# Performance work log

Hardware: AMD Instinct MI355X
Metric: run time of the kernel (lower is better)

## Reference

```python
import jax, jax.numpy as jnp
import numpy as np

B, T, C, H = 2, 2048, 1024, 16
D = C // H  # head dim = 64


def setup_inputs() -> dict:
    key = jax.random.key(0)
    ks = jax.random.split(key, 9)
    s = 1.0 / np.sqrt(C)
    x = jax.random.normal(ks[0], (B, T, C), dtype=jnp.float32)
    # causal lower-triangular mask, broadcast over heads: [B, 1, T, T]
    attn_mask = jnp.broadcast_to(jnp.tril(jnp.ones((T, T), dtype=jnp.int32)), (B, 1, T, T))
    Wq = jax.random.normal(ks[1], (C, C), dtype=jnp.float32) * s
    Wk = jax.random.normal(ks[2], (C, C), dtype=jnp.float32) * s
    Wv = jax.random.normal(ks[3], (C, C), dtype=jnp.float32) * s
    Wo = jax.random.normal(ks[4], (C, C), dtype=jnp.float32) * s
    bq = jax.random.normal(ks[5], (C,), dtype=jnp.float32) * s
    bk = jax.random.normal(ks[6], (C,), dtype=jnp.float32) * s
    bv = jax.random.normal(ks[7], (C,), dtype=jnp.float32) * s
    bo = jax.random.normal(ks[8], (C,), dtype=jnp.float32) * s
    return {"x": x, "attn_mask": attn_mask, "Wq": Wq, "bq": bq, "Wk": Wk, "bk": bk,
            "Wv": Wv, "bv": bv, "Wo": Wo, "bo": bo}


def reference(x, attn_mask, Wq, bq, Wk, bk, Wv, bv, Wo, bo):
    # Q/K/V projections: nn.Linear applies x @ W^T + b
    def split_heads(t):  # [B,T,C] -> [B,H,T,D]
        return t.reshape(B, T, H, D).transpose(0, 2, 1, 3)

    q = split_heads(x @ Wq.T + bq)
    k = split_heads(x @ Wk.T + bk)
    v = split_heads(x @ Wv.T + bv)

    scale = 1.0 / np.sqrt(D)
    att = jnp.einsum('bhqd,bhkd->bhqk', q, k) * scale  # [B,H,T,T]
    att = jnp.where(attn_mask[:, :, :T, :T] == 0, -jnp.inf, att)
    att = jax.nn.softmax(att, axis=-1)
    # dropout p=0.0 -> identity
    y = jnp.einsum('bhqk,bhkd->bhqd', att, v)  # [B,H,T,D]
    y = y.transpose(0, 2, 1, 3).reshape(B, T, C)
    return y @ Wo.T + bo
```

## Files before the change

kernel.cpp:

```cpp
#include <hip/hip_runtime.h>
#include <hip/hip_bf16.h>

#define B_ 2
#define T_ 2048
#define C_ 1024
#define H_ 16
#define D_ 64
#define BT_ (B_ * T_)
#define S3_ 3072

typedef __bf16 bf16x8 __attribute__((ext_vector_type(8)));
typedef short short8 __attribute__((ext_vector_type(8)));
typedef float f32x4 __attribute__((ext_vector_type(4)));

__device__ inline bf16x8 ld_frag_bf(const short* p) {
    short8 s = *(const short8*)p;
    return __builtin_bit_cast(bf16x8, s);
}
__device__ inline short f2bf(float f) {
    union { float f; unsigned u; } x;
    x.f = f;
    unsigned r = x.u + 0x7fff + ((x.u >> 16) & 1);
    return (short)(r >> 16);
}
__device__ inline void st_out(short* p, float v) { *p = f2bf(v); }
__device__ inline void st_out(float* p, float v) { *p = v; }

__device__ inline void async16(const void* g, void* l) {
    __builtin_amdgcn_global_load_lds(
        (const __attribute__((address_space(1))) unsigned*)g,
        (__attribute__((address_space(3))) unsigned*)l, 16, 0, 0);
}

__global__ __launch_bounds__(256) void conv_inputs(
    const float* __restrict__ x,
    const float* __restrict__ Wq, const float* __restrict__ Wk,
    const float* __restrict__ Wv, const float* __restrict__ Wo,
    short* __restrict__ xb, short* __restrict__ Wqkvb, short* __restrict__ Wob)
{
    size_t e = ((size_t)blockIdx.x * 256 + threadIdx.x) * 8;
    int r = (int)(e >> 20);
    size_t off = e & ((1u << 20) - 1);
    const float* src; short* dst;
    if (r < 4)      { src = x + e;  dst = xb + e; }
    else if (r < 7) { src = (r == 4 ? Wq : r == 5 ? Wk : Wv) + off;
                      dst = Wqkvb + ((size_t)(r - 4) << 20) + off; }
    else            { src = Wo + off; dst = Wob + off; }
    f32x4 a = *(const f32x4*)src;
    f32x4 b = *(const f32x4*)(src + 4);
    short8 s;
#pragma unroll
    for (int i = 0; i < 4; ++i) { s[i] = f2bf(a[i]); s[i + 4] = f2bf(b[i]); }
    *(short8*)dst = s;
}

template <typename OT>
__global__ __launch_bounds__(256) void gemm_m97(
    const short* __restrict__ A, int lda,
    const short* __restrict__ Wb,
    const float* __restrict__ b0, const float* __restrict__ b1,
    const float* __restrict__ b2,
    OT* __restrict__ Out, int ldo)
{
    constexpr int K = 1024;
    __shared__ __align__(16) short Bs[128 * 32];
    __shared__ __align__(16) short As[128 * 32];

    const int tid = threadIdx.x;
    const int w = tid >> 6, l = tid & 63;
    const int c = l & 15, qd = l >> 4;
    const int m0 = blockIdx.y * 128, n0 = blockIdx.x * 128;
    const int wm = w >> 1, wn = w & 1;

    const float* bias = (n0 < 1024) ? b0 : (n0 < 2048 ? b1 : b2);

    f32x4 acc[4][4] = {};

    for (int k0 = 0; k0 < K; k0 += 32) {
#pragma unroll
        for (int p = 0; p < 2; ++p) {
            int row = p * 64 + w * 16 + (l >> 2);
            async16(Wb + (size_t)(n0 + row) * K + k0 + (l & 3) * 8,
                    Bs + p * 2048 + w * 512 + l * 8);
            async16(A + (size_t)(m0 + row) * lda + k0 + (l & 3) * 8,
                    As + p * 2048 + w * 512 + l * 8);
        }
        __syncthreads();

        bf16x8 af[4], bfr[4];
#pragma unroll
        for (int i = 0; i < 4; ++i) {
            af[i]  = ld_frag_bf(As + (wm * 64 + i * 16 + c) * 32 + qd * 8);
            bfr[i] = ld_frag_bf(Bs + (wn * 64 + i * 16 + c) * 32 + qd * 8);
        }
#pragma unroll
        for (int i = 0; i < 4; ++i)
#pragma unroll
            for (int j = 0; j < 4; ++j)
                acc[i][j] = __builtin_amdgcn_mfma_f32_16x16x32_bf16(af[i], bfr[j], acc[i][j], 0, 0, 0);
        __syncthreads();
    }

#pragma unroll
    for (int i = 0; i < 4; ++i)
#pragma unroll
        for (int j = 0; j < 4; ++j) {
            int n = n0 + wn * 64 + j * 16 + c;
            float bv = bias[n & 1023];
#pragma unroll
            for (int r = 0; r < 4; ++r) {
                int m = m0 + wm * 64 + i * 16 + qd * 4 + r;
                st_out(Out + (size_t)m * ldo + n, acc[i][j][r] + bv);
            }
        }
}

__global__ __launch_bounds__(256) void attn_flash4(short* __restrict__ QKV)
{
    __shared__ __align__(16) short Ksm[2][64 * 64];
    __shared__ __align__(16) short Vsm[2][64 * 72];
    __shared__ __align__(16) short Psm[4][16 * 72];

    const int tid = threadIdx.x;
    const int w = tid >> 6, l = tid & 63;
    const int c = l & 15, qd = l >> 4;
    const int pair = blockIdx.x;
    const int bh = blockIdx.y;
    const int b = bh >> 4, h = bh & 15;
    const int sw = c & 7;

    short* Qbase = QKV + (size_t)b * T_ * S3_ + h * 64;
    const short* Kbase = Qbase + 1024;
    const short* Vbase = Qbase + 2048;

#pragma unroll 1
    for (int seg = 0; seg < 2; ++seg) {
        const int qt = (seg == 0) ? pair : 31 - pair;
        const int q0 = qt * 64, wq0 = q0 + w * 16;

        bf16x8 aq0 = ld_frag_bf(Qbase + (size_t)(wq0 + c) * S3_ + qd * 8);
        bf16x8 aq1 = ld_frag_bf(Qbase + (size_t)(wq0 + c) * S3_ + 32 + qd * 8);

        f32x4 o[4] = {};
        float lrow[4] = {0.f, 0.f, 0.f, 0.f};

        {
#pragma unroll
            for (int p = 0; p < 2; ++p) {
                int row = p * 32 + w * 8 + (l >> 3);
                int srcC = (l & 7) ^ (row & 7);
                async16(Kbase + (size_t)row * S3_ + srcC * 8,
                        &Ksm[0][row * 64 + (l & 7) * 8]);
            }
            const short* g = Vbase + (size_t)l * S3_ + w * 16;
            short8 v0 = *(const short8*)g;
            short8 v1 = *(const short8*)(g + 8);
#pragma unroll
            for (int e = 0; e < 8; ++e) {
                Vsm[0][(w * 16 + e) * 72 + l]     = v0[e];
                Vsm[0][(w * 16 + 8 + e) * 72 + l] = v1[e];
            }
        }
        __syncthreads();

#pragma unroll 1
        for (int kt = 0; kt <= qt; ++kt) {
            const int cur = kt & 1;
            const int k0 = kt * 64;

            short8 nv0, nv1;
            if (kt < qt) {
#pragma unroll
                for (int p = 0; p < 2; ++p) {
                    int row = p * 32 + w * 8 + (l >> 3);
                    int srcC = (l & 7) ^ (row & 7);
                    async16(Kbase + (size_t)(k0 + 64 + row) * S3_ + srcC * 8,
                            &Ksm[1 - cur][row * 64 + (l & 7) * 8]);
                }
                const short* g = Vbase + (size_t)(k0 + 64 + l) * S3_ + w * 16;
                nv0 = *(const short8*)g;
                nv1 = *(const short8*)(g + 8);
            }

            f32x4 s[4];
#pragma unroll
            for (int j = 0; j < 4; ++j) {
                s[j] = (f32x4){0.f, 0.f, 0.f, 0.f};
                const short* kr = &Ksm[cur][(j * 16 + c) * 64];
                bf16x8 kb0 = ld_frag_bf(kr + (qd ^ sw) * 8);
                bf16x8 kb1 = ld_frag_bf(kr + (qd ^ 4 ^ sw) * 8);
                s[j] = __builtin_amdgcn_mfma_f32_16x16x32_bf16(aq0, kb0, s[j], 0, 0, 0);
                s[j] = __builtin_amdgcn_mfma_f32_16x16x32_bf16(aq1, kb1, s[j], 0, 0, 0);
            }

            const bool diag = (kt == qt);
            float p_[4][4];
#pragma unroll
            for (int r = 0; r < 4; ++r) {
                const int qrow = wq0 + qd * 4 + r;
                float acc = 0.f;
#pragma unroll
                for (int j = 0; j < 4; ++j) {
                    float p = __expf(fmaf(s[j][r], 0.125f, -8.0f));
                    if (diag && (k0 + j * 16 + c > qrow)) p = 0.f;
                    p_[r][j] = p;
                    acc += p;
                }
                lrow[r] += acc;
            }

            short* P = Psm[w];
#pragma unroll
            for (int r = 0; r < 4; ++r)
#pragma unroll
                for (int j = 0; j < 4; ++j)
                    P[(qd * 4 + r) * 72 + j * 16 + c] = f2bf(p_[r][j]);

            if (kt < qt) {
#pragma unroll
                for (int e = 0; e < 8; ++e) {
                    Vsm[1 - cur][(w * 16 + e) * 72 + l]     = nv0[e];
                    Vsm[1 - cur][(w * 16 + 8 + e) * 72 + l] = nv1[e];
                }
            }

            bf16x8 pa0 = ld_frag_bf(P + c * 72 + qd * 8);
            bf16x8 pa1 = ld_frag_bf(P + c * 72 + 32 + qd * 8);
#pragma unroll
            for (int j = 0; j < 4; ++j) {
                bf16x8 vb0 = ld_frag_bf(&Vsm[cur][(j * 16 + c) * 72 + qd * 8]);
                bf16x8 vb1 = ld_frag_bf(&Vsm[cur][(j * 16 + c) * 72 + 32 + qd * 8]);
                o[j] = __builtin_amdgcn_mfma_f32_16x16x32_bf16(pa0, vb0, o[j], 0, 0, 0);
                o[j] = __builtin_amdgcn_mfma_f32_16x16x32_bf16(pa1, vb1, o[j], 0, 0, 0);
            }
            __syncthreads();
        }

        float inv[4];
#pragma unroll
        for (int r = 0; r < 4; ++r) {
            float s = lrow[r];
            s += __shfl_xor(s, 1);
            s += __shfl_xor(s, 2);
            s += __shfl_xor(s, 4);
            s += __shfl_xor(s, 8);
            inv[r] = 1.0f / s;
        }

#pragma unroll
        for (int j = 0; j < 4; ++j)
#pragma unroll
            for (int r = 0; r < 4; ++r) {
                int qrow = wq0 + qd * 4 + r;
                Qbase[(size_t)qrow * S3_ + j * 16 + c] = f2bf(o[j][r] * inv[r]);
            }
    }
}

extern "C" void kernel_launch(void* const* d_in, const int* in_sizes, int n_in,
                              void* d_out, int out_size, void* d_ws, size_t ws_size,
                              hipStream_t stream)
{
    const float* x  = (const float*)d_in[0];
    const float* Wq = (const float*)d_in[2];
    const float* bq = (const float*)d_in[3];
    const float* Wk = (const float*)d_in[4];
    const float* bk = (const float*)d_in[5];
    const float* Wv = (const float*)d_in[6];
    const float* bv = (const float*)d_in[7];
    const float* Wo = (const float*)d_in[8];
    const float* bo = (const float*)d_in[9];
    float* out = (float*)d_out;

    short* QKVs  = (short*)d_ws;
    short* Wqkvb = QKVs + (size_t)BT_ * S3_;
    short* Wob   = Wqkvb + (size_t)S3_ * C_;
    short* xb    = (short*)d_out;

    conv_inputs<<<4096, 256, 0, stream>>>(x, Wq, Wk, Wv, Wo, xb, Wqkvb, Wob);
    gemm_m97<short><<<dim3(S3_ / 128, BT_ / 128), 256, 0, stream>>>(
        xb, C_, Wqkvb, bq, bk, bv, QKVs, S3_);
    attn_flash4<<<dim3(16, B_ * H_), 256, 0, stream>>>(QKVs);
    gemm_m97<float><<<dim3(C_ / 128, BT_ / 128), 256, 0, stream>>>(
        QKVs, S3_, Wob, bo, bo, bo, out, C_);
}
```

Baseline: 227.6 us.

## Pre-transpose V, async-load it in attention, split mask path, retile output GEMM

A new kernel writes V in a transposed layout to a scratch area inside the output buffer. The attention kernel can then load V tiles with async 16-byte copies into swizzled shared memory, replacing the register-staged scatter transpose it did on every tile. The kernel also uses a remapped 1-D grid to group heads, and evaluates the causal mask only on the diagonal tile. The output projection moves to a new 128x64-tile GEMM, which doubles its block count, at the cost of one extra launch and an extra pass over V.

Measured after the change: 210.4 us. -7.5%, faster.

```diff
diff --git a/kernel.cpp b/kernel.cpp
--- a/kernel.cpp
+++ b/kernel.cpp
@@ -115,28 +115,122 @@
         }
 }
 
-__global__ __launch_bounds__(256) void attn_flash4(short* __restrict__ QKV)
-{
-    __shared__ __align__(16) short Ksm[2][64 * 64];
-    __shared__ __align__(16) short Vsm[2][64 * 72];
-    __shared__ __align__(16) short Psm[4][16 * 72];
+template <typename OT>
+__global__ __launch_bounds__(256) void gemm_n64(
+    const short* __restrict__ A, int lda,
+    const short* __restrict__ Wb, const float* __restrict__ bias,
+    OT* __restrict__ Out, int ldo)
+{
+    constexpr int K = 1024;
+    __shared__ __align__(16) short Bs[64 * 32];
+    __shared__ __align__(16) short As[128 * 32];
 
     const int tid = threadIdx.x;
     const int w = tid >> 6, l = tid & 63;
     const int c = l & 15, qd = l >> 4;
-    const int pair = blockIdx.x;
-    const int bh = blockIdx.y;
+    const int m0 = blockIdx.y * 128, n0 = blockIdx.x * 64;
+    const int wm = w >> 1, wn = w & 1;
+
+    f32x4 acc[4][2] = {};
+
+    for (int k0 = 0; k0 < K; k0 += 32) {
+        {
+            int row = w * 16 + (l >> 2);
+            async16(Wb + (size_t)(n0 + row) * K + k0 + (l & 3) * 8,
+                    Bs + w * 512 + l * 8);
+        }
+#pragma unroll
+        for (int p = 0; p < 2; ++p) {
+            int row = p * 64 + w * 16 + (l >> 2);
+            async16(A + (size_t)(m0 + row) * lda + k0 + (l & 3) * 8,
+                    As + p * 2048 + w * 512 + l * 8);
+        }
+        __syncthreads();
+
+        bf16x8 af[4], bfr[2];
+#pragma unroll
+        for (int i = 0; i < 4; ++i)
+            af[i] = ld_frag_bf(As + (wm * 64 + i * 16 + c) * 32 + qd * 8);
+#pragma unroll
+        for (int j = 0; j < 2; ++j)
+            bfr[j] = ld_frag_bf(Bs + (wn * 32 + j * 16 + c) * 32 + qd * 8);
+#pragma unroll
+        for (int i = 0; i < 4; ++i)
+#pragma unroll
+            for (int j = 0; j < 2; ++j)
+                acc[i][j] = __builtin_amdgcn_mfma_f32_16x16x32_bf16(af[i], bfr[j], acc[i][j], 0, 0, 0);
+        __syncthreads();
+    }
+
+#pragma unroll
+    for (int i = 0; i < 4; ++i)
+#pragma unroll
+        for (int j = 0; j < 2; ++j) {
+            int n = n0 + wn * 32 + j * 16 + c;
+            float bv = bias[n];
+#pragma unroll
+            for (int r = 0; r < 4; ++r) {
+                int m = m0 + wm * 64 + i * 16 + qd * 4 + r;
+                st_out(Out + (size_t)m * ldo + n, acc[i][j][r] + bv);
+            }
+        }
+}
+
+__global__ __launch_bounds__(256) void transpose_v(
+    const short* __restrict__ QKV, short* __restrict__ VT)
+{
+    __shared__ short Tm[64 * 80];
+    const int t = threadIdx.x;
+    const int kt = blockIdx.x, bh = blockIdx.y;
+    const int b = bh >> 4, h = bh & 15;
+    const short* Vg = QKV + (size_t)b * T_ * S3_ + 2048 + h * 64;
+
+    {
+        int key = t >> 2, dc = (t & 3) * 16;
+        const short* g = Vg + (size_t)(kt * 64 + key) * S3_ + dc;
+        short8 a = *(const short8*)g;
+        short8 c8 = *(const short8*)(g + 8);
+#pragma unroll
+        for (int e = 0; e < 8; ++e) {
+            Tm[(dc + e) * 80 + key]     = a[e];
+            Tm[(dc + 8 + e) * 80 + key] = c8[e];
+        }
+    }
+    __syncthreads();
+    {
+        int d = t >> 2, kc = (t & 3) * 16;
+        short8 w0 = *(const short8*)&Tm[d * 80 + kc];
+        short8 w1 = *(const short8*)&Tm[d * 80 + kc + 8];
+        short* o = VT + ((size_t)bh * 64 + d) * T_ + kt * 64 + kc;
+        *(short8*)o = w0;
+        *(short8*)(o + 8) = w1;
+    }
+}
+
+__global__ __launch_bounds__(256) void attn_flash5(
+    short* __restrict__ QKV, const short* __restrict__ VT)
+{
+    __shared__ __align__(16) short Ksm[2][64 * 64];
+    __shared__ __align__(16) short Vsm[2][64 * 64];
+    __shared__ __align__(16) short Psm[4][16 * 72];
+
+    const int tid = threadIdx.x;
+    const int w = tid >> 6, l = tid & 63;
+    const int c = l & 15, qd = l >> 4;
+    const int id = blockIdx.x;
+    const int bh = (id & 7) * 4 + ((id >> 3) & 3);
+    const int pair = id >> 5;
     const int b = bh >> 4, h = bh & 15;
     const int sw = c & 7;
 
     short* Qbase = QKV + (size_t)b * T_ * S3_ + h * 64;
     const short* Kbase = Qbase + 1024;
-    const short* Vbase = Qbase + 2048;
+    const short* VTb = VT + (size_t)bh * 64 * T_;
 
 #pragma unroll 1
     for (int seg = 0; seg < 2; ++seg) {
-        const int qt = (seg == 0) ? pair : 31 - pair;
-        const int q0 = qt * 64, wq0 = q0 + w * 16;
+        const int qt = seg ? (31 - pair) : pair;
+        const int wq0 = qt * 64 + w * 16;
 
         bf16x8 aq0 = ld_frag_bf(Qbase + (size_t)(wq0 + c) * S3_ + qd * 8);
         bf16x8 aq1 = ld_frag_bf(Qbase + (size_t)(wq0 + c) * S3_ + 32 + qd * 8);
@@ -144,22 +238,14 @@
         f32x4 o[4] = {};
         float lrow[4] = {0.f, 0.f, 0.f, 0.f};
 
-        {
-#pragma unroll
-            for (int p = 0; p < 2; ++p) {
-                int row = p * 32 + w * 8 + (l >> 3);
-                int srcC = (l & 7) ^ (row & 7);
-                async16(Kbase + (size_t)row * S3_ + srcC * 8,
-                        &Ksm[0][row * 64 + (l & 7) * 8]);
-            }
-            const short* g = Vbase + (size_t)l * S3_ + w * 16;
-            short8 v0 = *(const short8*)g;
-            short8 v1 = *(const short8*)(g + 8);
-#pragma unroll
-            for (int e = 0; e < 8; ++e) {
-                Vsm[0][(w * 16 + e) * 72 + l]     = v0[e];
-                Vsm[0][(w * 16 + 8 + e) * 72 + l] = v1[e];
-            }
+#pragma unroll
+        for (int p = 0; p < 2; ++p) {
+            int row = p * 32 + w * 8 + (l >> 3);
+            int srcC = (l & 7) ^ (row & 7);
+            async16(Kbase + (size_t)row * S3_ + srcC * 8,
+                    &Ksm[0][row * 64 + (l & 7) * 8]);
+            async16(VTb + (size_t)row * T_ + srcC * 8,
+                    &Vsm[0][row * 64 + (l & 7) * 8]);
         }
         __syncthreads();
 
@@ -168,7 +254,6 @@
             const int cur = kt & 1;
             const int k0 = kt * 64;
 
-            short8 nv0, nv1;
             if (kt < qt) {
 #pragma unroll
                 for (int p = 0; p < 2; ++p) {
@@ -176,10 +261,9 @@
                     int srcC = (l & 7) ^ (row & 7);
                     async16(Kbase + (size_t)(k0 + 64 + row) * S3_ + srcC * 8,
                             &Ksm[1 - cur][row * 64 + (l & 7) * 8]);
+                    async16(VTb + (size_t)row * T_ + k0 + 64 + srcC * 8,
+                            &Vsm[1 - cur][row * 64 + (l & 7) * 8]);
                 }
-                const short* g = Vbase + (size_t)(k0 + 64 + l) * S3_ + w * 16;
-                nv0 = *(const short8*)g;
-                nv1 = *(const short8*)(g + 8);
             }
 
             f32x4 s[4];
@@ -188,25 +272,38 @@
                 s[j] = (f32x4){0.f, 0.f, 0.f, 0.f};
                 const short* kr = &Ksm[cur][(j * 16 + c) * 64];
                 bf16x8 kb0 = ld_frag_bf(kr + (qd ^ sw) * 8);
-                bf16x8 kb1 = ld_frag_bf(kr + (qd ^ 4 ^ sw) * 8);
+                bf16x8 kb1 = ld_frag_bf(kr + ((qd ^ 4) ^ sw) * 8);
                 s[j] = __builtin_amdgcn_mfma_f32_16x16x32_bf16(aq0, kb0, s[j], 0, 0, 0);
                 s[j] = __builtin_amdgcn_mfma_f32_16x16x32_bf16(aq1, kb1, s[j], 0, 0, 0);
             }
 
-            const bool diag = (kt == qt);
             float p_[4][4];
-#pragma unroll
-            for (int r = 0; r < 4; ++r) {
-                const int qrow = wq0 + qd * 4 + r;
-                float acc = 0.f;
-#pragma unroll
-                for (int j = 0; j < 4; ++j) {
-                    float p = __expf(fmaf(s[j][r], 0.125f, -8.0f));
-                    if (diag && (k0 + j * 16 + c > qrow)) p = 0.f;
-                    p_[r][j] = p;
-                    acc += p;
+            if (kt < qt) {
+#pragma unroll
+                for (int r = 0; r < 4; ++r) {
+                    float acc = 0.f;
+#pragma unroll
+                    for (int j = 0; j < 4; ++j) {
+                        float p = __expf(fmaf(s[j][r], 0.125f, -8.0f));
+                        p_[r][j] = p;
+                        acc += p;
+                    }
+                    lrow[r] += acc;
                 }
-                lrow[r] += acc;
+            } else {
+#pragma unroll
+                for (int r = 0; r < 4; ++r) {
+                    const int qrow = wq0 + qd * 4 + r;
+                    float acc = 0.f;
+#pragma unroll
+                    for (int j = 0; j < 4; ++j) {
+                        float p = __expf(fmaf(s[j][r], 0.125f, -8.0f));
+                        if (k0 + j * 16 + c > qrow) p = 0.f;
+                        p_[r][j] = p;
+                        acc += p;
+                    }
+                    lrow[r] += acc;
+                }
             }
 
             short* P = Psm[w];
@@ -216,20 +313,13 @@
                 for (int j = 0; j < 4; ++j)
                     P[(qd * 4 + r) * 72 + j * 16 + c] = f2bf(p_[r][j]);
 
-            if (kt < qt) {
-#pragma unroll
-                for (int e = 0; e < 8; ++e) {
-                    Vsm[1 - cur][(w * 16 + e) * 72 + l]     = nv0[e];
-                    Vsm[1 - cur][(w * 16 + 8 + e) * 72 + l] = nv1[e];
-                }
-            }
-
             bf16x8 pa0 = ld_frag_bf(P + c * 72 + qd * 8);
             bf16x8 pa1 = ld_frag_bf(P + c * 72 + 32 + qd * 8);
 #pragma unroll
             for (int j = 0; j < 4; ++j) {
-                bf16x8 vb0 = ld_frag_bf(&Vsm[cur][(j * 16 + c) * 72 + qd * 8]);
-                bf16x8 vb1 = ld_frag_bf(&Vsm[cur][(j * 16 + c) * 72 + 32 + qd * 8]);
+                const short* vr = &Vsm[cur][(j * 16 + c) * 64];
+                bf16x8 vb0 = ld_frag_bf(vr + (qd ^ sw) * 8);
+                bf16x8 vb1 = ld_frag_bf(vr + ((qd ^ 4) ^ sw) * 8);
                 o[j] = __builtin_amdgcn_mfma_f32_16x16x32_bf16(pa0, vb0, o[j], 0, 0, 0);
                 o[j] = __builtin_amdgcn_mfma_f32_16x16x32_bf16(pa1, vb1, o[j], 0, 0, 0);
             }
@@ -276,11 +366,13 @@
     short* Wqkvb = QKVs + (size_t)BT_ * S3_;
     short* Wob   = Wqkvb + (size_t)S3_ * C_;
     short* xb    = (short*)d_out;
+    short* VT    = (short*)d_out + (size_t)4 * 1024 * 1024;
 
     conv_inputs<<<4096, 256, 0, stream>>>(x, Wq, Wk, Wv, Wo, xb, Wqkvb, Wob);
     gemm_m97<short><<<dim3(S3_ / 128, BT_ / 128), 256, 0, stream>>>(
         xb, C_, Wqkvb, bq, bk, bv, QKVs, S3_);
-    attn_flash4<<<dim3(16, B_ * H_), 256, 0, stream>>>(QKVs);
-    gemm_m97<float><<<dim3(C_ / 128, BT_ / 128), 256, 0, stream>>>(
-        QKVs, S3_, Wob, bo, bo, bo, out, C_);
-}
+    transpose_v<<<dim3(T_ / 64, B_ * H_), 256, 0, stream>>>(QKVs, VT);
+    attn_flash5<<<512, 256, 0, stream>>>(QKVs, VT);
+    gemm_n64<float><<<dim3(C_ / 64, BT_ / 128), 256, 0, stream>>>(
+        QKVs, S3_, Wob, bo, out, C_);
+}
```
